# Kernel optimization log

Measured on AMD Instinct MI355X. Metric: run time of the kernel, lower is better.

The kernel has to match this reference:

```python
import jax, jax.numpy as jnp
import numpy as np

N_NODES = 100000
N_EDGES = 600000
D_IN = 128
D_OUT = 128


def setup_inputs() -> dict:
    key = jax.random.key(0)
    k1, k2, k3 = jax.random.split(key, 3)
    x = jax.random.normal(k1, (N_NODES, D_IN), dtype=jnp.float32)
    edge_index = jax.random.randint(k2, (2, N_EDGES), 0, N_NODES, dtype=jnp.int64)
    # Glorot-style init for the GCN weight, zero bias (PyG defaults)
    W = jax.random.normal(k3, (D_IN, D_OUT), dtype=jnp.float32) * (1.0 / np.sqrt(D_IN))
    b = jnp.zeros((D_OUT,), dtype=jnp.float32)
    return {"x": x, "edge_index": edge_index, "W": W, "b": b}


def reference(x, edge_index, W, b):
    """GCNConv: out = D^{-1/2} (A + I) D^{-1/2} (x @ W) + b."""
    n = x.shape[0]
    self_loop = jnp.arange(n, dtype=edge_index.dtype)
    src = jnp.concatenate([edge_index[0], self_loop])  # [E + N]
    dst = jnp.concatenate([edge_index[1], self_loop])

    xw = x @ W  # [N, D_OUT] dense transform before aggregation

    # symmetric normalization with self-loops
    deg = jax.ops.segment_sum(jnp.ones_like(dst, dtype=x.dtype), dst, num_segments=n)
    dinv = jnp.where(deg > 0, jax.lax.rsqrt(deg), 0.0)
    norm = dinv[src] * dinv[dst]  # [E + N]

    # gather source features, scale, scatter-add to destinations
    msgs = norm[:, None] * xw[src]  # [E + N, D_OUT]
    out = jax.ops.segment_sum(msgs, dst, num_segments=n)
    return out + b
```

## Files before the change

kernel.cpp:

```cpp
#include <hip/hip_runtime.h>
#include <hip/hip_bf16.h>
#include <stdint.h>

#define N_NODES 100000
#define N_EDGES 600000
#define D 128
#define WT2 72
#define SCAN_NBLK ((N_NODES + 255) / 256)
#define CAP 32

typedef unsigned short u16;
typedef uint32_t u32;
typedef __attribute__((ext_vector_type(8))) short bf16x8;
typedef __attribute__((ext_vector_type(4))) float f32x4;

union bfpack { bf16x8 v; u16 s[8]; };

__device__ __forceinline__ float bf2f(u16 u) {
    union { u32 i; float f; } v; v.i = ((u32)u) << 16; return v.f;
}
__device__ __forceinline__ u16 f2bf(float f) {
    union { float f; u32 i; } v; v.f = f;
    u32 lsb = (v.i >> 16) & 1u;
    return (u16)((v.i + 0x7fffu + lsb) >> 16);
}


__global__ __launch_bounds__(256) void k_init(const u32* __restrict__ xu,
                                              const int* __restrict__ ei,
                                              int* __restrict__ deg,
                                              int* __restrict__ flags) {
    int t = threadIdx.x;
    int idx = blockIdx.x * 256 + t;
    if (idx < N_NODES) deg[idx] = 0;
    if (blockIdx.x == 0) {
        __shared__ int cnt[2];
        if (t < 2) cnt[t] = 0;
        __syncthreads();
        const u32* eu = (const u32*)ei;
        int bad = 0, zc = 0;
        for (int i = 0; i < 16; i++) {
            u32 w = xu[t + 256 * i];
            int e0 = (w >> 7) & 0xFF, e1 = (w >> 23) & 0xFF;
            bad += ((e0 == 0 || e0 == 0xFF) ? 1 : 0) + ((e1 == 0 || e1 == 0xFF) ? 1 : 0);
            zc += (eu[2 * (t + 256 * i) + 1] == 0) ? 1 : 0;
        }
        atomicAdd(&cnt[0], bad);
        atomicAdd(&cnt[1], zc);
        __syncthreads();
        if (t == 0) { flags[0] = cnt[0] > 8 ? 1 : 0; flags[1] = cnt[1] > 2048 ? 1 : 0; }
    }
}

__global__ __launch_bounds__(256) void k_prep(const int* __restrict__ flags,
                                              const void* __restrict__ Wp,
                                              u16* __restrict__ wthi,
                                              u16* __restrict__ wtlo) {
    int t = blockIdx.x * 256 + threadIdx.x;
    if (flags[0]) {
        const float* Wf = (const float*)Wp;
        for (int i = 0; i < 8; i++) {
            int idx = t + i * 2048;
            float w = Wf[idx];
            int k = idx >> 7, n = idx & 127;
            u16 h = f2bf(w);
            wthi[n * 128 + k] = h;
            wtlo[n * 128 + k] = f2bf(w - bf2f(h));
        }
    } else {
        const u16* W16 = (const u16*)Wp;
        for (int i = 0; i < 8; i++) {
            int idx = t + i * 2048;
            int k = idx >> 7, n = idx & 127;
            wthi[n * 128 + k] = W16[idx];
        }
    }
}

__global__ __launch_bounds__(256) void k_build(const int* __restrict__ ei,
                                               const int* __restrict__ flags,
                                               int* __restrict__ cnt,
                                               int* __restrict__ csr) {
    int e = blockIdx.x * 256 + threadIdx.x;
    if (e >= N_EDGES) return;
    int s, d;
    if (flags[1]) { s = ei[2 * e]; d = ei[2 * (N_EDGES + e)]; }
    else          { s = ei[e];     d = ei[N_EDGES + e]; }
    if ((unsigned)s >= N_NODES) s = 0;
    if ((unsigned)d >= N_NODES) d = 0;
    int slot = atomicAdd(&cnt[d], 1);
    if (slot < CAP)
        csr[((long)(slot >> 2) * N_NODES + d) * 4 + (slot & 3)] = s;
}

__global__ void k_hist(const int* __restrict__ ei, const int* __restrict__ flags,
                       int* __restrict__ deg) {
    int e = blockIdx.x * 256 + threadIdx.x;
    if (e < N_EDGES) {
        int d = flags[1] ? ei[2 * (N_EDGES + e)] : ei[N_EDGES + e];
        if ((unsigned)d >= N_NODES) d = 0;
        atomicAdd(&deg[d], 1);
    }
}

__global__ __launch_bounds__(256) void k_reduce(const int* __restrict__ deg,
                                                int* __restrict__ bsum) {
    __shared__ int ws[4];
    int t = threadIdx.x, lane = t & 63, wave = t >> 6;
    int idx = blockIdx.x * 256 + t;
    int v = (idx < N_NODES) ? deg[idx] : 0;
    for (int o = 32; o > 0; o >>= 1) v += __shfl_down(v, o, 64);
    if (lane == 0) ws[wave] = v;
    __syncthreads();
    if (t == 0) bsum[blockIdx.x] = ws[0] + ws[1] + ws[2] + ws[3];
}

__global__ __launch_bounds__(512) void k_scanbs(const int* __restrict__ bsum,
                                                int* __restrict__ bpre,
                                                int* __restrict__ offs) {
    __shared__ int lds[512];
    int t = threadIdx.x;
    int v = (t < SCAN_NBLK) ? bsum[t] : 0;
    lds[t] = v;
    __syncthreads();
    for (int off = 1; off < 512; off <<= 1) {
        int u = (t >= off) ? lds[t - off] : 0;
        __syncthreads();
        lds[t] += u;
        __syncthreads();
    }
    if (t < SCAN_NBLK) bpre[t] = (t == 0) ? 0 : lds[t - 1];
    if (t == SCAN_NBLK - 1) offs[N_NODES] = lds[t];
}

__global__ __launch_bounds__(256) void k_apply(const int* __restrict__ deg,
                                               const int* __restrict__ bpre,
                                               int* __restrict__ offs,
                                               int* __restrict__ cursor) {
    __shared__ int ws[4];
    int t = threadIdx.x, lane = t & 63, wave = t >> 6;
    int idx = blockIdx.x * 256 + t;
    int d = (idx < N_NODES) ? deg[idx] : 0;
    int v = d;
    for (int o = 1; o < 64; o <<= 1) {
        int u = __shfl_up(v, o, 64);
        if (lane >= o) v += u;
    }
    if (lane == 63) ws[wave] = v;
    __syncthreads();
    int add = 0;
    for (int w = 0; w < wave; w++) add += ws[w];
    int excl = bpre[blockIdx.x] + add + v - d;
    if (idx < N_NODES) {
        offs[idx] = excl;
        cursor[idx] = excl;
    }
}

__global__ void k_scatter(const int* __restrict__ ei, const int* __restrict__ flags,
                          int* __restrict__ cursor, int* __restrict__ csr) {
    int e = blockIdx.x * 256 + threadIdx.x;
    if (e < N_EDGES) {
        int s, d;
        if (flags[1]) { s = ei[2 * e]; d = ei[2 * (N_EDGES + e)]; }
        else          { s = ei[e];     d = ei[N_EDGES + e]; }
        if ((unsigned)s >= N_NODES) s = 0;
        if ((unsigned)d >= N_NODES) d = 0;
        int slot = atomicAdd(&cursor[d], 1);
        csr[slot] = s;
    }
}

__global__ __launch_bounds__(256, 3) void k_gemm(const int* __restrict__ flags,
                                                 const void* __restrict__ xp,
                                                 const u16* __restrict__ wthi,
                                                 const u16* __restrict__ wtlo,
                                                 const int* __restrict__ deg,
                                                 u16* __restrict__ xw) {
    __shared__ u16 Wlds[2][128 * WT2];
    int t = threadIdx.x, wave = t >> 6, lane = t & 63;
    int m16 = lane & 15, q = lane >> 4;
    int row0 = blockIdx.x * 128 + wave * 32;
    f32x4 acc[2][8];
    for (int a = 0; a < 2; a++)
        for (int c = 0; c < 8; c++) acc[a][c] = (f32x4){0.f, 0.f, 0.f, 0.f};

    int r0 = row0 + m16;      if (r0 > N_NODES - 1) r0 = N_NODES - 1;
    int r1 = row0 + 16 + m16; if (r1 > N_NODES - 1) r1 = N_NODES - 1;

    if (flags[0]) {
        const float* xf = (const float*)xp;
#pragma unroll
        for (int kh = 0; kh < 2; kh++) {
            float4 xr[8];
#pragma unroll
            for (int kt = 0; kt < 2; kt++) {
                int kg = kh * 64 + kt * 32 + q * 8;
                xr[kt * 4 + 0] = *(const float4*)(xf + (long)r0 * D + kg);
                xr[kt * 4 + 1] = *(const float4*)(xf + (long)r0 * D + kg + 4);
                xr[kt * 4 + 2] = *(const float4*)(xf + (long)r1 * D + kg);
                xr[kt * 4 + 3] = *(const float4*)(xf + (long)r1 * D + kg + 4);
            }
            if (kh) __syncthreads();
#pragma unroll
            for (int i = 0; i < 8; i++) {
                int idx = i * 256 + t;
                int arr = idx >> 10;
                int r = (idx >> 3) & 127;
                int c8 = idx & 7;
                const u16* src = (arr ? wtlo : wthi) + r * 128 + kh * 64 + c8 * 8;
                *(bf16x8*)&Wlds[arr][r * WT2 + c8 * 8] = *(const bf16x8*)src;
            }
            __syncthreads();
#pragma unroll
            for (int kt = 0; kt < 2; kt++) {
                int kl = kt * 32 + q * 8;
                float t0[8] = {xr[kt * 4 + 0].x, xr[kt * 4 + 0].y, xr[kt * 4 + 0].z, xr[kt * 4 + 0].w,
                               xr[kt * 4 + 1].x, xr[kt * 4 + 1].y, xr[kt * 4 + 1].z, xr[kt * 4 + 1].w};
                float t1[8] = {xr[kt * 4 + 2].x, xr[kt * 4 + 2].y, xr[kt * 4 + 2].z, xr[kt * 4 + 2].w,
                               xr[kt * 4 + 3].x, xr[kt * 4 + 3].y, xr[kt * 4 + 3].z, xr[kt * 4 + 3].w};
                bfpack h0, l0, h1, l1;
#pragma unroll
                for (int j = 0; j < 8; j++) {
                    u16 a = f2bf(t0[j]); h0.s[j] = a; l0.s[j] = f2bf(t0[j] - bf2f(a));
                    u16 b = f2bf(t1[j]); h1.s[j] = b; l1.s[j] = f2bf(t1[j] - bf2f(b));
                }
#pragma unroll
                for (int ct = 0; ct < 8; ct++) {
                    bf16x8 bh = *(const bf16x8*)(&Wlds[0][(ct * 16 + m16) * WT2 + kl]);
                    bf16x8 bl = *(const bf16x8*)(&Wlds[1][(ct * 16 + m16) * WT2 + kl]);
                    acc[0][ct] = __builtin_amdgcn_mfma_f32_16x16x32_bf16(h0.v, bh, acc[0][ct], 0, 0, 0);
                    acc[0][ct] = __builtin_amdgcn_mfma_f32_16x16x32_bf16(l0.v, bh, acc[0][ct], 0, 0, 0);
                    acc[0][ct] = __builtin_amdgcn_mfma_f32_16x16x32_bf16(h0.v, bl, acc[0][ct], 0, 0, 0);
                    acc[1][ct] = __builtin_amdgcn_mfma_f32_16x16x32_bf16(h1.v, bh, acc[1][ct], 0, 0, 0);
                    acc[1][ct] = __builtin_amdgcn_mfma_f32_16x16x32_bf16(l1.v, bh, acc[1][ct], 0, 0, 0);
                    acc[1][ct] = __builtin_amdgcn_mfma_f32_16x16x32_bf16(h1.v, bl, acc[1][ct], 0, 0, 0);
                }
            }
        }
    } else {
        const u16* x16 = (const u16*)xp;
        bf16x8 wb[8][4];
#pragma unroll
        for (int ct = 0; ct < 8; ct++)
#pragma unroll
            for (int kt = 0; kt < 4; kt++)
                wb[ct][kt] = *(const bf16x8*)(wthi + (ct * 16 + m16) * 128 + kt * 32 + q * 8);
        bf16x8 a0[4], a1[4];
#pragma unroll
        for (int kt = 0; kt < 4; kt++) {
            int kbase = kt * 32 + q * 8;
            a0[kt] = *(const bf16x8*)(x16 + (long)r0 * D + kbase);
            a1[kt] = *(const bf16x8*)(x16 + (long)r1 * D + kbase);
        }
#pragma unroll
        for (int kt = 0; kt < 4; kt++)
#pragma unroll
            for (int ct = 0; ct < 8; ct++) {
                acc[0][ct] = __builtin_amdgcn_mfma_f32_16x16x32_bf16(a0[kt], wb[ct][kt], acc[0][ct], 0, 0, 0);
                acc[1][ct] = __builtin_amdgcn_mfma_f32_16x16x32_bf16(a1[kt], wb[ct][kt], acc[1][ct], 0, 0, 0);
            }
    }
    for (int a = 0; a < 2; a++)
        for (int r = 0; r < 4; r++) {
            int row = row0 + a * 16 + q * 4 + r;
            if (row < N_NODES) {
                float dr = rsqrtf((float)(deg[row] + 1));
                for (int ct = 0; ct < 8; ct++)
                    xw[(long)row * D + ct * 16 + m16] = f2bf(dr * acc[a][ct][r]);
            }
        }
}

__global__ __launch_bounds__(256) void k_agg_bkt(const int* __restrict__ flags,
                                                 const u16* __restrict__ xw,
                                                 const int* __restrict__ csr,
                                                 const int* __restrict__ cnt,
                                                 const void* __restrict__ bp,
                                                 void* __restrict__ outp) {
    int t = threadIdx.x;
    int wave = t >> 6, lane = t & 63;
    int g = lane >> 4, i = lane & 15;
    int nb = blockIdx.x * 16 + wave * 4;
    int n = nb + g;

    int4 dv = *(const int4*)(cnt + nb);
    int deg = (g == 0) ? dv.x : (g == 1) ? dv.y : (g == 2) ? dv.z : dv.w;
    float dn = rsqrtf((float)(deg + 1));
    int m = deg < CAP ? deg : CAP;
    int P = (m <= 8) ? 8 : ((m + 3) & ~3);
    float padf = (float)(1 - (P - m));

    const u16* xwc = xw + i * 8;
    int4 q0 = *(const int4*)(csr + (long)n * 4);
    int4 q1 = *(const int4*)(csr + ((long)N_NODES + n) * 4);
    bfpack pv; pv.v = *(const bf16x8*)(xwc + (long)n * D);

    int s0 = (0 < m) ? q0.x : n, s1 = (1 < m) ? q0.y : n;
    int s2 = (2 < m) ? q0.z : n, s3 = (3 < m) ? q0.w : n;
    int s4 = (4 < m) ? q1.x : n, s5 = (5 < m) ? q1.y : n;
    int s6 = (6 < m) ? q1.z : n, s7 = (7 < m) ? q1.w : n;
    bfpack g0, g1, g2, g3, g4, g5, g6, g7;
    g0.v = *(const bf16x8*)(xwc + (long)s0 * D);
    g1.v = *(const bf16x8*)(xwc + (long)s1 * D);
    g2.v = *(const bf16x8*)(xwc + (long)s2 * D);
    g3.v = *(const bf16x8*)(xwc + (long)s3 * D);
    g4.v = *(const bf16x8*)(xwc + (long)s4 * D);
    g5.v = *(const bf16x8*)(xwc + (long)s5 * D);
    g6.v = *(const bf16x8*)(xwc + (long)s6 * D);
    g7.v = *(const bf16x8*)(xwc + (long)s7 * D);

    float ax[8];
#pragma unroll
    for (int j2 = 0; j2 < 8; j2++) {
        ax[j2] = bf2f(pv.s[j2]) * padf +
                 ((bf2f(g0.s[j2]) + bf2f(g1.s[j2])) + (bf2f(g2.s[j2]) + bf2f(g3.s[j2]))) +
                 ((bf2f(g4.s[j2]) + bf2f(g5.s[j2])) + (bf2f(g6.s[j2]) + bf2f(g7.s[j2])));
    }

    for (int j = 8; j < m; j += 4) {
        int4 qi = *(const int4*)(csr + ((long)(j >> 2) * N_NODES + n) * 4);
        int t0 = qi.x;
        int t1 = (j + 1 < m) ? qi.y : n;
        int t2 = (j + 2 < m) ? qi.z : n;
        int t3 = (j + 3 < m) ? qi.w : n;
        bfpack h0, h1, h2, h3;
        h0.v = *(const bf16x8*)(xwc + (long)t0 * D);
        h1.v = *(const bf16x8*)(xwc + (long)t1 * D);
        h2.v = *(const bf16x8*)(xwc + (long)t2 * D);
        h3.v = *(const bf16x8*)(xwc + (long)t3 * D);
#pragma unroll
        for (int j2 = 0; j2 < 8; j2++)
            ax[j2] += (bf2f(h0.s[j2]) + bf2f(h1.s[j2])) +
                      (bf2f(h2.s[j2]) + bf2f(h3.s[j2]));
    }

    if (flags[0]) {
        const float* bf_ = (const float*)bp;
        f32x4 b0 = *(const f32x4*)(bf_ + i * 8);
        f32x4 b1 = *(const f32x4*)(bf_ + i * 8 + 4);
        f32x4 o0, o1;
#pragma unroll
        for (int j2 = 0; j2 < 4; j2++) {
            o0[j2] = dn * ax[j2] + b0[j2];
            o1[j2] = dn * ax[j2 + 4] + b1[j2];
        }
        float* outf = (float*)outp;
        *(f32x4*)(outf + (long)n * D + i * 8) = o0;
        *(f32x4*)(outf + (long)n * D + i * 8 + 4) = o1;
    } else {
        const u16* b16 = (const u16*)bp;
        bfpack bb; bb.v = *(const bf16x8*)(b16 + i * 8);
        bfpack ob;
#pragma unroll
        for (int j2 = 0; j2 < 8; j2++) ob.s[j2] = f2bf(dn * ax[j2] + bf2f(bb.s[j2]));
        u16* out16 = (u16*)outp;
        *(bf16x8*)(out16 + (long)n * D + i * 8) = ob.v;
    }
}

__global__ __launch_bounds__(256) void k_agg_csr(const int* __restrict__ flags,
                                                 const u16* __restrict__ xw,
                                                 const int* __restrict__ csr,
                                                 const int* __restrict__ offs,
                                                 const void* __restrict__ bp,
                                                 void* __restrict__ outp) {
    int wave = threadIdx.x >> 6, lane = threadIdx.x & 63;
    int n = blockIdx.x * 4 + wave;
    int c = lane * 2;
    int e0 = offs[n], e1 = offs[n + 1];
    float dn = rsqrtf((float)(e1 - e0 + 1));
    u32 pv = *(const u32*)(xw + (long)n * D + c);
    float ax = bf2f((u16)pv), ay = bf2f((u16)(pv >> 16));
    int j = e0;
    for (; j + 4 <= e1; j += 4) {
        int s0 = csr[j], s1 = csr[j + 1], s2 = csr[j + 2], s3 = csr[j + 3];
        u32 q0 = *(const u32*)(xw + (long)s0 * D + c);
        u32 q1 = *(const u32*)(xw + (long)s1 * D + c);
        u32 q2 = *(const u32*)(xw + (long)s2 * D + c);
        u32 q3 = *(const u32*)(xw + (long)s3 * D + c);
        ax += bf2f((u16)q0) + bf2f((u16)q1) + bf2f((u16)q2) + bf2f((u16)q3);
        ay += bf2f((u16)(q0 >> 16)) + bf2f((u16)(q1 >> 16)) +
              bf2f((u16)(q2 >> 16)) + bf2f((u16)(q3 >> 16));
    }
    for (; j < e1; j++) {
        int s = csr[j];
        u32 qv = *(const u32*)(xw + (long)s * D + c);
        ax += bf2f((u16)qv);
        ay += bf2f((u16)(qv >> 16));
    }
    if (flags[0]) {
        const float* bf_ = (const float*)bp;
        float2 bb = *(const float2*)(bf_ + c);
        float* outf = (float*)outp;
        *(float2*)(outf + (long)n * D + c) = make_float2(dn * ax + bb.x, dn * ay + bb.y);
    } else {
        const u16* b16 = (const u16*)bp;
        u32 bb = *(const u32*)(b16 + c);
        u16* out16 = (u16*)outp;
        u32 o = (u32)f2bf(dn * ax + bf2f((u16)bb)) |
                ((u32)f2bf(dn * ay + bf2f((u16)(bb >> 16))) << 16);
        *(u32*)(out16 + (long)n * D + c) = o;
    }
}

extern "C" void kernel_launch(void* const* d_in, const int* in_sizes, int n_in,
                              void* d_out, int out_size, void* d_ws, size_t ws_size,
                              hipStream_t stream) {
    const void* x  = d_in[0];
    const int* ei  = (const int*)d_in[1];
    const void* W  = d_in[2];
    const void* b  = d_in[3];
    char* ws = (char*)d_ws;

    const size_t BUCKET_NEED = 38865664 + 64;
    if (ws_size >= BUCKET_NEED) {
        int* flags = (int*)(ws + 0);
        int* cnt   = (int*)(ws + 64);
        int* csr   = (int*)(ws + 400128);
        u16* xw    = (u16*)(ws + 13200128);
        u16* wthi  = (u16*)(ws + 38800128);
        u16* wtlo  = (u16*)(ws + 38832896);
        k_init<<<SCAN_NBLK, 256, 0, stream>>>((const u32*)x, ei, cnt, flags);
        k_build<<<(N_EDGES + 255) / 256, 256, 0, stream>>>(ei, flags, cnt, csr);
        k_prep<<<8, 256, 0, stream>>>(flags, W, wthi, wtlo);
        k_gemm<<<(N_NODES + 127) / 128, 256, 0, stream>>>(flags, x, wthi, wtlo, cnt, xw);
        k_agg_bkt<<<N_NODES / 16, 256, 0, stream>>>(flags, xw, csr, cnt, b, d_out);
    } else {
        int*   flags  = (int*)(ws + 0);
        int*   deg    = (int*)(ws + 64);
        int*   offs   = (int*)(ws + 400064);
        int*   cursor = (int*)(ws + 800068);
        int*   csr    = (int*)(ws + 1200068);
        int*   bsum   = (int*)(ws + 3600068);
        int*   bpre   = (int*)(ws + 3601636);
        u16*   xw     = (u16*)(ws + 3603216);
        u16*   wthi   = (u16*)(ws + 29203264);
        u16*   wtlo   = (u16*)(ws + 29236032);
        k_init<<<SCAN_NBLK, 256, 0, stream>>>((const u32*)x, ei, deg, flags);
        k_hist<<<(N_EDGES + 255) / 256, 256, 0, stream>>>(ei, flags, deg);
        k_reduce<<<SCAN_NBLK, 256, 0, stream>>>(deg, bsum);
        k_scanbs<<<1, 512, 0, stream>>>(bsum, bpre, offs);
        k_apply<<<SCAN_NBLK, 256, 0, stream>>>(deg, bpre, offs, cursor);
        k_prep<<<8, 256, 0, stream>>>(flags, W, wthi, wtlo);
        k_gemm<<<(N_NODES + 127) / 128, 256, 0, stream>>>(flags, x, wthi, wtlo, deg, xw);
        k_scatter<<<(N_EDGES + 255) / 256, 256, 0, stream>>>(ei, flags, cursor, csr);
        k_agg_csr<<<N_NODES / 4, 256, 0, stream>>>(flags, xw, csr, offs, b, d_out);
    }
}
```

Before: 186.6 us.

## Fuse bucket CSR build into GEMM kernel, move source-degree scaling into aggregation

Folds the edge-bucketing pass (atomic degree count plus CSR slot write) into the GEMM kernel, with each block handling 768 edges before its matmul, which removes one kernel launch. Because degrees are no longer final when xw is written, the per-row dinv[src] scaling moves out of the GEMM epilogue. The aggregation kernels now load cnt[src] for every neighbour and apply an rsqrt on it. This adds extra random gathers and rsqrt work in exchange for the launch saved and possible overlap of atomics with GEMM memory traffic.

```diff
diff --git a/kernel.cpp b/kernel.cpp
--- a/kernel.cpp
+++ b/kernel.cpp
@@ -8,6 +8,7 @@
 #define WT2 72
 #define SCAN_NBLK ((N_NODES + 255) / 256)
 #define CAP 32
+#define GEMM_NBLK ((N_NODES + 127) / 128)
 
 typedef unsigned short u16;
 typedef uint32_t u32;
@@ -77,22 +78,6 @@
     }
 }
 
-__global__ __launch_bounds__(256) void k_build(const int* __restrict__ ei,
-                                               const int* __restrict__ flags,
-                                               int* __restrict__ cnt,
-                                               int* __restrict__ csr) {
-    int e = blockIdx.x * 256 + threadIdx.x;
-    if (e >= N_EDGES) return;
-    int s, d;
-    if (flags[1]) { s = ei[2 * e]; d = ei[2 * (N_EDGES + e)]; }
-    else          { s = ei[e];     d = ei[N_EDGES + e]; }
-    if ((unsigned)s >= N_NODES) s = 0;
-    if ((unsigned)d >= N_NODES) d = 0;
-    int slot = atomicAdd(&cnt[d], 1);
-    if (slot < CAP)
-        csr[((long)(slot >> 2) * N_NODES + d) * 4 + (slot & 3)] = s;
-}
-
 __global__ void k_hist(const int* __restrict__ ei, const int* __restrict__ flags,
                        int* __restrict__ deg) {
     int e = blockIdx.x * 256 + threadIdx.x;
@@ -171,16 +156,35 @@
     }
 }
 
-__global__ __launch_bounds__(256, 3) void k_gemm(const int* __restrict__ flags,
-                                                 const void* __restrict__ xp,
-                                                 const u16* __restrict__ wthi,
-                                                 const u16* __restrict__ wtlo,
-                                                 const int* __restrict__ deg,
-                                                 u16* __restrict__ xw) {
+__global__ __launch_bounds__(256, 3) void k_fused(const int* __restrict__ flags,
+                                                  const void* __restrict__ xp,
+                                                  const u16* __restrict__ wthi,
+                                                  const u16* __restrict__ wtlo,
+                                                  const int* __restrict__ ei,
+                                                  int* __restrict__ cnt,
+                                                  int* __restrict__ csr,
+                                                  u16* __restrict__ xw) {
     __shared__ u16 Wlds[2][128 * WT2];
     int t = threadIdx.x, wave = t >> 6, lane = t & 63;
     int m16 = lane & 15, q = lane >> 4;
     int row0 = blockIdx.x * 128 + wave * 32;
+
+    int f64 = flags[1];
+#pragma unroll
+    for (int i = 0; i < 3; i++) {
+        int e = blockIdx.x * 768 + i * 256 + t;
+        if (e < N_EDGES) {
+            int s, d;
+            if (f64) { s = ei[2 * e]; d = ei[2 * (N_EDGES + e)]; }
+            else     { s = ei[e];     d = ei[N_EDGES + e]; }
+            if ((unsigned)s >= N_NODES) s = 0;
+            if ((unsigned)d >= N_NODES) d = 0;
+            int slot = atomicAdd(&cnt[d], 1);
+            if (slot < CAP)
+                csr[((long)(slot >> 2) * N_NODES + d) * 4 + (slot & 3)] = s;
+        }
+    }
+
     f32x4 acc[2][8];
     for (int a = 0; a < 2; a++)
         for (int c = 0; c < 8; c++) acc[a][c] = (f32x4){0.f, 0.f, 0.f, 0.f};
@@ -264,11 +268,105 @@
     for (int a = 0; a < 2; a++)
         for (int r = 0; r < 4; r++) {
             int row = row0 + a * 16 + q * 4 + r;
-            if (row < N_NODES) {
-                float dr = rsqrtf((float)(deg[row] + 1));
+            if (row < N_NODES)
                 for (int ct = 0; ct < 8; ct++)
-                    xw[(long)row * D + ct * 16 + m16] = f2bf(dr * acc[a][ct][r]);
-            }
+                    xw[(long)row * D + ct * 16 + m16] = f2bf(acc[a][ct][r]);
+        }
+}
+
+__global__ __launch_bounds__(256, 3) void k_gemm(const int* __restrict__ flags,
+                                                 const void* __restrict__ xp,
+                                                 const u16* __restrict__ wthi,
+                                                 const u16* __restrict__ wtlo,
+                                                 u16* __restrict__ xw) {
+    __shared__ u16 Wlds[2][128 * WT2];
+    int t = threadIdx.x, wave = t >> 6, lane = t & 63;
+    int m16 = lane & 15, q = lane >> 4;
+    int row0 = blockIdx.x * 128 + wave * 32;
+    f32x4 acc[2][8];
+    for (int a = 0; a < 2; a++)
+        for (int c = 0; c < 8; c++) acc[a][c] = (f32x4){0.f, 0.f, 0.f, 0.f};
+    int r0 = row0 + m16;      if (r0 > N_NODES - 1) r0 = N_NODES - 1;
+    int r1 = row0 + 16 + m16; if (r1 > N_NODES - 1) r1 = N_NODES - 1;
+    if (flags[0]) {
+        const float* xf = (const float*)xp;
+#pragma unroll
+        for (int kh = 0; kh < 2; kh++) {
+            float4 xr[8];
+#pragma unroll
+            for (int kt = 0; kt < 2; kt++) {
+                int kg = kh * 64 + kt * 32 + q * 8;
+                xr[kt * 4 + 0] = *(const float4*)(xf + (long)r0 * D + kg);
+                xr[kt * 4 + 1] = *(const float4*)(xf + (long)r0 * D + kg + 4);
+                xr[kt * 4 + 2] = *(const float4*)(xf + (long)r1 * D + kg);
+                xr[kt * 4 + 3] = *(const float4*)(xf + (long)r1 * D + kg + 4);
+            }
+            if (kh) __syncthreads();
+#pragma unroll
+            for (int i = 0; i < 8; i++) {
+                int idx = i * 256 + t;
+                int arr = idx >> 10;
+                int r = (idx >> 3) & 127;
+                int c8 = idx & 7;
+                const u16* src = (arr ? wtlo : wthi) + r * 128 + kh * 64 + c8 * 8;
+                *(bf16x8*)&Wlds[arr][r * WT2 + c8 * 8] = *(const bf16x8*)src;
+            }
+            __syncthreads();
+#pragma unroll
+            for (int kt = 0; kt < 2; kt++) {
+                int kl = kt * 32 + q * 8;
+                float t0[8] = {xr[kt * 4 + 0].x, xr[kt * 4 + 0].y, xr[kt * 4 + 0].z, xr[kt * 4 + 0].w,
+                               xr[kt * 4 + 1].x, xr[kt * 4 + 1].y, xr[kt * 4 + 1].z, xr[kt * 4 + 1].w};
+                float t1[8] = {xr[kt * 4 + 2].x, xr[kt * 4 + 2].y, xr[kt * 4 + 2].z, xr[kt * 4 + 2].w,
+                               xr[kt * 4 + 3].x, xr[kt * 4 + 3].y, xr[kt * 4 + 3].z, xr[kt * 4 + 3].w};
+                bfpack h0, l0, h1, l1;
+#pragma unroll
+                for (int j = 0; j < 8; j++) {
+                    u16 a = f2bf(t0[j]); h0.s[j] = a; l0.s[j] = f2bf(t0[j] - bf2f(a));
+                    u16 b = f2bf(t1[j]); h1.s[j] = b; l1.s[j] = f2bf(t1[j] - bf2f(b));
+                }
+#pragma unroll
+                for (int ct = 0; ct < 8; ct++) {
+                    bf16x8 bh = *(const bf16x8*)(&Wlds[0][(ct * 16 + m16) * WT2 + kl]);
+                    bf16x8 bl = *(const bf16x8*)(&Wlds[1][(ct * 16 + m16) * WT2 + kl]);
+                    acc[0][ct] = __builtin_amdgcn_mfma_f32_16x16x32_bf16(h0.v, bh, acc[0][ct], 0, 0, 0);
+                    acc[0][ct] = __builtin_amdgcn_mfma_f32_16x16x32_bf16(l0.v, bh, acc[0][ct], 0, 0, 0);
+                    acc[0][ct] = __builtin_amdgcn_mfma_f32_16x16x32_bf16(h0.v, bl, acc[0][ct], 0, 0, 0);
+                    acc[1][ct] = __builtin_amdgcn_mfma_f32_16x16x32_bf16(h1.v, bh, acc[1][ct], 0, 0, 0);
+                    acc[1][ct] = __builtin_amdgcn_mfma_f32_16x16x32_bf16(l1.v, bh, acc[1][ct], 0, 0, 0);
+                    acc[1][ct] = __builtin_amdgcn_mfma_f32_16x16x32_bf16(h1.v, bl, acc[1][ct], 0, 0, 0);
+                }
+            }
+        }
+    } else {
+        const u16* x16 = (const u16*)xp;
+        bf16x8 wb[8][4];
+#pragma unroll
+        for (int ct = 0; ct < 8; ct++)
+#pragma unroll
+            for (int kt = 0; kt < 4; kt++)
+                wb[ct][kt] = *(const bf16x8*)(wthi + (ct * 16 + m16) * 128 + kt * 32 + q * 8);
+        bf16x8 a0[4], a1[4];
+#pragma unroll
+        for (int kt = 0; kt < 4; kt++) {
+            int kbase = kt * 32 + q * 8;
+            a0[kt] = *(const bf16x8*)(x16 + (long)r0 * D + kbase);
+            a1[kt] = *(const bf16x8*)(x16 + (long)r1 * D + kbase);
+        }
+#pragma unroll
+        for (int kt = 0; kt < 4; kt++)
+#pragma unroll
+            for (int ct = 0; ct < 8; ct++) {
+                acc[0][ct] = __builtin_amdgcn_mfma_f32_16x16x32_bf16(a0[kt], wb[ct][kt], acc[0][ct], 0, 0, 0);
+                acc[1][ct] = __builtin_amdgcn_mfma_f32_16x16x32_bf16(a1[kt], wb[ct][kt], acc[1][ct], 0, 0, 0);
+            }
+    }
+    for (int a = 0; a < 2; a++)
+        for (int r = 0; r < 4; r++) {
+            int row = row0 + a * 16 + q * 4 + r;
+            if (row < N_NODES)
+                for (int ct = 0; ct < 8; ct++)
+                    xw[(long)row * D + ct * 16 + m16] = f2bf(acc[a][ct][r]);
         }
 }
 
@@ -285,9 +383,9 @@
     int n = nb + g;
 
     int4 dv = *(const int4*)(cnt + nb);
-    int deg = (g == 0) ? dv.x : (g == 1) ? dv.y : (g == 2) ? dv.z : dv.w;
-    float dn = rsqrtf((float)(deg + 1));
-    int m = deg < CAP ? deg : CAP;
+    int degn = (g == 0) ? dv.x : (g == 1) ? dv.y : (g == 2) ? dv.z : dv.w;
+    float wn = rsqrtf((float)(degn + 1));
+    int m = degn < CAP ? degn : CAP;
     int P = (m <= 8) ? 8 : ((m + 3) & ~3);
     float padf = (float)(1 - (P - m));
 
@@ -300,6 +398,8 @@
     int s2 = (2 < m) ? q0.z : n, s3 = (3 < m) ? q0.w : n;
     int s4 = (4 < m) ? q1.x : n, s5 = (5 < m) ? q1.y : n;
     int s6 = (6 < m) ? q1.z : n, s7 = (7 < m) ? q1.w : n;
+    int d0 = cnt[s0], d1 = cnt[s1], d2 = cnt[s2], d3 = cnt[s3];
+    int d4 = cnt[s4], d5 = cnt[s5], d6 = cnt[s6], d7 = cnt[s7];
     bfpack g0, g1, g2, g3, g4, g5, g6, g7;
     g0.v = *(const bf16x8*)(xwc + (long)s0 * D);
     g1.v = *(const bf16x8*)(xwc + (long)s1 * D);
@@ -309,13 +409,19 @@
     g5.v = *(const bf16x8*)(xwc + (long)s5 * D);
     g6.v = *(const bf16x8*)(xwc + (long)s6 * D);
     g7.v = *(const bf16x8*)(xwc + (long)s7 * D);
+    float w0 = rsqrtf((float)(d0 + 1)), w1 = rsqrtf((float)(d1 + 1));
+    float w2 = rsqrtf((float)(d2 + 1)), w3 = rsqrtf((float)(d3 + 1));
+    float w4 = rsqrtf((float)(d4 + 1)), w5 = rsqrtf((float)(d5 + 1));
+    float w6 = rsqrtf((float)(d6 + 1)), w7 = rsqrtf((float)(d7 + 1));
 
     float ax[8];
 #pragma unroll
     for (int j2 = 0; j2 < 8; j2++) {
-        ax[j2] = bf2f(pv.s[j2]) * padf +
-                 ((bf2f(g0.s[j2]) + bf2f(g1.s[j2])) + (bf2f(g2.s[j2]) + bf2f(g3.s[j2]))) +
-                 ((bf2f(g4.s[j2]) + bf2f(g5.s[j2])) + (bf2f(g6.s[j2]) + bf2f(g7.s[j2])));
+        ax[j2] = padf * wn * bf2f(pv.s[j2]) +
+                 ((w0 * bf2f(g0.s[j2]) + w1 * bf2f(g1.s[j2])) +
+                  (w2 * bf2f(g2.s[j2]) + w3 * bf2f(g3.s[j2]))) +
+                 ((w4 * bf2f(g4.s[j2]) + w5 * bf2f(g5.s[j2])) +
+                  (w6 * bf2f(g6.s[j2]) + w7 * bf2f(g7.s[j2])));
     }
 
     for (int j = 8; j < m; j += 4) {
@@ -324,6 +430,8 @@
         int t1 = (j + 1 < m) ? qi.y : n;
         int t2 = (j + 2 < m) ? qi.z : n;
         int t3 = (j + 3 < m) ? qi.w : n;
+        float u0 = rsqrtf((float)(cnt[t0] + 1)), u1 = rsqrtf((float)(cnt[t1] + 1));
+        float u2 = rsqrtf((float)(cnt[t2] + 1)), u3 = rsqrtf((float)(cnt[t3] + 1));
         bfpack h0, h1, h2, h3;
         h0.v = *(const bf16x8*)(xwc + (long)t0 * D);
         h1.v = *(const bf16x8*)(xwc + (long)t1 * D);
@@ -331,8 +439,8 @@
         h3.v = *(const bf16x8*)(xwc + (long)t3 * D);
 #pragma unroll
         for (int j2 = 0; j2 < 8; j2++)
-            ax[j2] += (bf2f(h0.s[j2]) + bf2f(h1.s[j2])) +
-                      (bf2f(h2.s[j2]) + bf2f(h3.s[j2]));
+            ax[j2] += (u0 * bf2f(h0.s[j2]) + u1 * bf2f(h1.s[j2])) +
+                      (u2 * bf2f(h2.s[j2]) + u3 * bf2f(h3.s[j2]));
     }
 
     if (flags[0]) {
@@ -342,8 +450,8 @@
         f32x4 o0, o1;
 #pragma unroll
         for (int j2 = 0; j2 < 4; j2++) {
-            o0[j2] = dn * ax[j2] + b0[j2];
-            o1[j2] = dn * ax[j2 + 4] + b1[j2];
+            o0[j2] = wn * ax[j2] + b0[j2];
+            o1[j2] = wn * ax[j2 + 4] + b1[j2];
         }
         float* outf = (float*)outp;
         *(f32x4*)(outf + (long)n * D + i * 8) = o0;
@@ -353,7 +461,7 @@
         bfpack bb; bb.v = *(const bf16x8*)(b16 + i * 8);
         bfpack ob;
 #pragma unroll
-        for (int j2 = 0; j2 < 8; j2++) ob.s[j2] = f2bf(dn * ax[j2] + bf2f(bb.s[j2]));
+        for (int j2 = 0; j2 < 8; j2++) ob.s[j2] = f2bf(wn * ax[j2] + bf2f(bb.s[j2]));
         u16* out16 = (u16*)outp;
         *(bf16x8*)(out16 + (long)n * D + i * 8) = ob.v;
     }
@@ -363,6 +471,7 @@
                                                  const u16* __restrict__ xw,
                                                  const int* __restrict__ csr,
                                                  const int* __restrict__ offs,
+                                                 const int* __restrict__ deg,
                                                  const void* __restrict__ bp,
                                                  void* __restrict__ outp) {
     int wave = threadIdx.x >> 6, lane = threadIdx.x & 63;
@@ -371,23 +480,13 @@
     int e0 = offs[n], e1 = offs[n + 1];
     float dn = rsqrtf((float)(e1 - e0 + 1));
     u32 pv = *(const u32*)(xw + (long)n * D + c);
-    float ax = bf2f((u16)pv), ay = bf2f((u16)(pv >> 16));
-    int j = e0;
-    for (; j + 4 <= e1; j += 4) {
-        int s0 = csr[j], s1 = csr[j + 1], s2 = csr[j + 2], s3 = csr[j + 3];
-        u32 q0 = *(const u32*)(xw + (long)s0 * D + c);
-        u32 q1 = *(const u32*)(xw + (long)s1 * D + c);
-        u32 q2 = *(const u32*)(xw + (long)s2 * D + c);
-        u32 q3 = *(const u32*)(xw + (long)s3 * D + c);
-        ax += bf2f((u16)q0) + bf2f((u16)q1) + bf2f((u16)q2) + bf2f((u16)q3);
-        ay += bf2f((u16)(q0 >> 16)) + bf2f((u16)(q1 >> 16)) +
-              bf2f((u16)(q2 >> 16)) + bf2f((u16)(q3 >> 16));
-    }
-    for (; j < e1; j++) {
+    float ax = dn * bf2f((u16)pv), ay = dn * bf2f((u16)(pv >> 16));
+    for (int j = e0; j < e1; j++) {
         int s = csr[j];
+        float w = rsqrtf((float)(deg[s] + 1));
         u32 qv = *(const u32*)(xw + (long)s * D + c);
-        ax += bf2f((u16)qv);
-        ay += bf2f((u16)(qv >> 16));
+        ax += w * bf2f((u16)qv);
+        ay += w * bf2f((u16)(qv >> 16));
     }
     if (flags[0]) {
         const float* bf_ = (const float*)bp;
@@ -422,9 +521,8 @@
         u16* wthi  = (u16*)(ws + 38800128);
         u16* wtlo  = (u16*)(ws + 38832896);
         k_init<<<SCAN_NBLK, 256, 0, stream>>>((const u32*)x, ei, cnt, flags);
-        k_build<<<(N_EDGES + 255) / 256, 256, 0, stream>>>(ei, flags, cnt, csr);
         k_prep<<<8, 256, 0, stream>>>(flags, W, wthi, wtlo);
-        k_gemm<<<(N_NODES + 127) / 128, 256, 0, stream>>>(flags, x, wthi, wtlo, cnt, xw);
+        k_fused<<<GEMM_NBLK, 256, 0, stream>>>(flags, x, wthi, wtlo, ei, cnt, csr, xw);
         k_agg_bkt<<<N_NODES / 16, 256, 0, stream>>>(flags, xw, csr, cnt, b, d_out);
     } else {
         int*   flags  = (int*)(ws + 0);
@@ -443,8 +541,8 @@
         k_scanbs<<<1, 512, 0, stream>>>(bsum, bpre, offs);
         k_apply<<<SCAN_NBLK, 256, 0, stream>>>(deg, bpre, offs, cursor);
         k_prep<<<8, 256, 0, stream>>>(flags, W, wthi, wtlo);
-        k_gemm<<<(N_NODES + 127) / 128, 256, 0, stream>>>(flags, x, wthi, wtlo, deg, xw);
+        k_gemm<<<(N_NODES + 127) / 128, 256, 0, stream>>>(flags, x, wthi, wtlo, xw);
         k_scatter<<<(N_EDGES + 255) / 256, 256, 0, stream>>>(ei, flags, cursor, csr);
-        k_agg_csr<<<N_NODES / 4, 256, 0, stream>>>(flags, xw, csr, offs, b, d_out);
-    }
-}
+        k_agg_csr<<<N_NODES / 4, 256, 0, stream>>>(flags, xw, csr, offs, deg, b, d_out);
+    }
+}
```

New measurement: 187.7 us. About the same (+0.6%).
